# Optimization experiments

Measured on AMD Instinct MI355X. Metric: run time of the kernel, lower is better.

The kernel has to match this reference:

```python
import jax, jax.numpy as jnp
import numpy as np

N_NODES = 50000
N_EDGES = 800000
IN_DIM = 128
HID = 128
N_GRAPHS = 64


def _sage_conv(x, src, dst, Wl, bl, Wr):
    # PyG SAGEConv (mean aggr): out = lin_l(mean_{j in N(i)} x_j) + lin_r(x_i)
    msg = x[src]                                            # [E, d] gather
    agg = jax.ops.segment_sum(msg, dst, num_segments=N_NODES)   # [N, d]
    deg = jax.ops.segment_sum(jnp.ones((msg.shape[0],), x.dtype), dst,
                              num_segments=N_NODES)          # [N]
    agg = agg / jnp.clip(deg, 1.0, None)[:, None]            # mean (0 for isolated)
    return agg @ Wl.T + bl + x @ Wr.T


def setup_inputs() -> dict:
    key = jax.random.key(0)
    ks = jax.random.split(key, 12)
    x = jax.random.normal(ks[0], (N_NODES, IN_DIM), dtype=jnp.float32)
    edge_index = jax.random.randint(ks[1], (2, N_EDGES), 0, N_NODES, dtype=jnp.int64)
    batch = jnp.sort(jax.random.randint(ks[2], (N_NODES,), 0, N_GRAPHS, dtype=jnp.int64))
    def lin(k, out_d, in_d):
        s = 1.0 / np.sqrt(in_d)
        return jax.random.uniform(k, (out_d, in_d), jnp.float32, -s, s)
    inp = {"x": x, "edge_index": edge_index, "batch": batch}
    dims = [(IN_DIM, HID), (HID, HID), (HID, HID)]
    for l, (din, dout) in enumerate(dims):
        inp[f"Wl{l}"] = lin(ks[3 + 3 * l], dout, din)
        inp[f"bl{l}"] = jnp.zeros((dout,), jnp.float32)
        inp[f"Wr{l}"] = lin(ks[4 + 3 * l], dout, din)
    return inp


def reference(x, edge_index, batch, Wl0, bl0, Wr0, Wl1, bl1, Wr1, Wl2, bl2, Wr2):
    src, dst = edge_index[0], edge_index[1]
    h = jax.nn.relu(_sage_conv(x, src, dst, Wl0, bl0, Wr0))
    h = jax.nn.relu(_sage_conv(h, src, dst, Wl1, bl1, Wr1))
    h = _sage_conv(h, src, dst, Wl2, bl2, Wr2)
    # global_mean_pool: segment mean of node features by graph id
    s = jax.ops.segment_sum(h, batch, num_segments=N_GRAPHS)        # [G, d]
    cnt = jax.ops.segment_sum(jnp.ones((h.shape[0],), h.dtype), batch,
                              num_segments=N_GRAPHS)                 # [G]
    return s / jnp.clip(cnt, 1.0, None)[:, None]
```

## Files before the change

### kernel.cpp

```cpp
#include <hip/hip_runtime.h>

#define N_NODES 50000
#define N_EDGES 800000
#define DIM 128
#define KTOT 256
#define N_GRAPHS 64
#define BUCKET_CAP 64
#define LSTR 264

#define NBINS 391
#define BINCAP2 2816
#define N_NODES_PAD (NBINS * 128)

#define BIN1_TPB 512
#define BIN1_EPT 8
#define BIN1_EPB (BIN1_TPB * BIN1_EPT)
#define BIN1_GRID ((N_EDGES + BIN1_EPB - 1) / BIN1_EPB)

typedef __attribute__((ext_vector_type(8))) short bf16x8;
typedef __attribute__((ext_vector_type(16))) float f32x16;

__device__ __forceinline__ float bf2f(unsigned int u16) {
    return __uint_as_float(u16 << 16);
}
__device__ __forceinline__ unsigned short f2bf(float f) {
    unsigned int v = __float_as_uint(f);
    unsigned int r = (v + 0x7fffu + ((v >> 16) & 1u)) >> 16;
    return (unsigned short)r;
}

__global__ void castx_kernel(const float* __restrict__ x, ushort* __restrict__ xb,
                             int* __restrict__ bincnt) {
    int i = blockIdx.x * blockDim.x + threadIdx.x;
    if (i < NBINS) bincnt[i] = 0;
    if (i >= N_NODES * DIM / 4) return;
    float4 v = ((const float4*)x)[i];
    ushort4 o;
    o.x = f2bf(v.x); o.y = f2bf(v.y); o.z = f2bf(v.z); o.w = f2bf(v.w);
    ((ushort4*)xb)[i] = o;
}

__global__ void castw_kernel(const float* __restrict__ Wl0, const float* __restrict__ Wr0,
                             const float* __restrict__ Wl1, const float* __restrict__ Wr1,
                             const float* __restrict__ Wl2, const float* __restrict__ Wr2,
                             ushort* __restrict__ wb, float* __restrict__ pool) {
    int id = blockIdx.x * blockDim.x + threadIdx.x;
    if (id < N_GRAPHS * DIM) pool[id] = 0.f;
    if (id >= 3 * DIM * KTOT) return;
    int l = id >> 15;
    int r = id & 32767;
    int j = r >> 8, k = r & 255;
    const float* Wl = (l == 0) ? Wl0 : (l == 1) ? Wl1 : Wl2;
    const float* Wr = (l == 0) ? Wr0 : (l == 1) ? Wr1 : Wr2;
    float v = (k < DIM) ? Wl[j * DIM + k] : Wr[j * DIM + k - DIM];
    wb[id] = f2bf(v);
}

__global__ __launch_bounds__(BIN1_TPB) void bin1_kernel(
    const int* __restrict__ src, const int* __restrict__ dst,
    int* __restrict__ bincnt, uint* __restrict__ binbuf) {
    __shared__ uint hist[NBINS];
    __shared__ uint gbase[NBINS];
    const int tid = threadIdx.x;
    for (int i = tid; i < NBINS; i += BIN1_TPB) hist[i] = 0;
    __syncthreads();

    const int e0 = blockIdx.x * BIN1_EPB + tid * BIN1_EPT;
    uint val[BIN1_EPT];
    int  bin[BIN1_EPT];
    uint rk[BIN1_EPT];

    if (e0 + BIN1_EPT <= N_EDGES) {
        int4 s0 = *(const int4*)(src + e0);
        int4 s1 = *(const int4*)(src + e0 + 4);
        int4 d0 = *(const int4*)(dst + e0);
        int4 d1 = *(const int4*)(dst + e0 + 4);
        int ss[8] = {s0.x, s0.y, s0.z, s0.w, s1.x, s1.y, s1.z, s1.w};
        int dd[8] = {d0.x, d0.y, d0.z, d0.w, d1.x, d1.y, d1.z, d1.w};
        #pragma unroll
        for (int i = 0; i < BIN1_EPT; ++i) {
            bin[i] = dd[i] >> 7;
            val[i] = (uint)ss[i] | ((uint)(dd[i] & 127) << 16);
            rk[i]  = atomicAdd(&hist[bin[i]], 1u);
        }
    } else {
        #pragma unroll
        for (int i = 0; i < BIN1_EPT; ++i) {
            if (e0 + i < N_EDGES) {
                int s = src[e0 + i], d = dst[e0 + i];
                bin[i] = d >> 7;
                val[i] = (uint)s | ((uint)(d & 127) << 16);
                rk[i]  = atomicAdd(&hist[bin[i]], 1u);
            } else {
                bin[i] = -1; val[i] = 0; rk[i] = 0;
            }
        }
    }
    __syncthreads();

    for (int i = tid; i < NBINS; i += BIN1_TPB)
        gbase[i] = (uint)atomicAdd(&bincnt[i], (int)hist[i]);
    __syncthreads();

    #pragma unroll
    for (int i = 0; i < BIN1_EPT; ++i) {
        if (bin[i] >= 0) {
            uint pos = gbase[bin[i]] + rk[i];
            if (pos < BINCAP2)
                binbuf[(size_t)bin[i] * BINCAP2 + pos] = val[i];
        }
    }
}

__global__ __launch_bounds__(256) void bin2_kernel(
    const uint* __restrict__ binbuf, const int* __restrict__ bincnt,
    ushort* __restrict__ bucket, int* __restrict__ cnt) {
    __shared__ int lcnt[128];
    __shared__ ushort lbuck[128 * BUCKET_CAP];
    const int bin = blockIdx.x;
    const int tid = threadIdx.x;
    if (tid < 128) lcnt[tid] = 0;
    __syncthreads();
    int c = bincnt[bin];
    if (c > BINCAP2) c = BINCAP2;
    const uint* buf = binbuf + (size_t)bin * BINCAP2;
    for (int i = tid; i < c; i += 256) {
        uint v = buf[i];
        int ln = v >> 16;
        int pos = atomicAdd(&lcnt[ln], 1);
        if (pos < BUCKET_CAP) lbuck[ln * BUCKET_CAP + pos] = (ushort)(v & 0xffffu);
    }
    __syncthreads();
    const uint4* lb = (const uint4*)lbuck;
    uint4* gb = (uint4*)(bucket + (size_t)bin * 128 * BUCKET_CAP);
    #pragma unroll
    for (int i = tid; i < 128 * BUCKET_CAP / 8; i += 256)
        gb[i] = lb[i];
    if (tid < 128) cnt[bin * 128 + tid] = lcnt[tid];
}

template<int RELU, int POOL>
__global__ __launch_bounds__(512, 4) void layer_fused(
    const ushort* __restrict__ X, const int* __restrict__ cnt,
    const ushort* __restrict__ bucket, const ushort* __restrict__ wb,
    const float* __restrict__ bl, ushort* __restrict__ outb,
    const int* __restrict__ batch, float* __restrict__ pool)
{
    __shared__ ushort sA[64 * LSTR];
    const int tid = threadIdx.x;
    const int lane = tid & 63, w = tid >> 6;
    const int mh = w & 1, jq = w >> 1;
    const int n0 = blockIdx.x * 64;
    const int half = lane >> 5, lcol = lane & 31;

    #pragma unroll
    for (int it = 0; it < 2; ++it) {
        int ci = tid + it * 512;
        int row = ci >> 4;
        int k8 = (ci & 15) * 8;
        int gn = n0 + row;
        bf16x8 v = (bf16x8){0,0,0,0,0,0,0,0};
        if (gn < N_NODES) v = *(const bf16x8*)(X + (size_t)gn * DIM + k8);
        *(bf16x8*)(&sA[row * LSTR + DIM + k8]) = v;
    }

    for (int r8 = 0; r8 < 8; ++r8) {
        const int row = w * 8 + r8;
        const int gn = n0 + row;
        float a0 = 0.f, a1 = 0.f, a2 = 0.f, a3 = 0.f;
        int c = 0;
        if (gn < N_NODES) {
            c = cnt[gn];
            int cl = c < BUCKET_CAP ? c : BUCKET_CAP;
            const ushort* b = bucket + (size_t)gn * BUCKET_CAP;
            int e = half;
            for (; e + 6 < cl; e += 8) {
                int s0 = b[e], s1 = b[e + 2], s2 = b[e + 4], s3 = b[e + 6];
                uint2 u0 = *(const uint2*)(X + (size_t)s0 * DIM + lcol * 4);
                uint2 u1 = *(const uint2*)(X + (size_t)s1 * DIM + lcol * 4);
                uint2 u2 = *(const uint2*)(X + (size_t)s2 * DIM + lcol * 4);
                uint2 u3 = *(const uint2*)(X + (size_t)s3 * DIM + lcol * 4);
                a0 += bf2f(u0.x & 0xffff) + bf2f(u1.x & 0xffff) + bf2f(u2.x & 0xffff) + bf2f(u3.x & 0xffff);
                a1 += bf2f(u0.x >> 16)    + bf2f(u1.x >> 16)    + bf2f(u2.x >> 16)    + bf2f(u3.x >> 16);
                a2 += bf2f(u0.y & 0xffff) + bf2f(u1.y & 0xffff) + bf2f(u2.y & 0xffff) + bf2f(u3.y & 0xffff);
                a3 += bf2f(u0.y >> 16)    + bf2f(u1.y >> 16)    + bf2f(u2.y >> 16)    + bf2f(u3.y >> 16);
            }
            for (; e < cl; e += 2) {
                int s0 = b[e];
                uint2 u0 = *(const uint2*)(X + (size_t)s0 * DIM + lcol * 4);
                a0 += bf2f(u0.x & 0xffff);
                a1 += bf2f(u0.x >> 16);
                a2 += bf2f(u0.y & 0xffff);
                a3 += bf2f(u0.y >> 16);
            }
        }
        a0 += __shfl_xor(a0, 32);
        a1 += __shfl_xor(a1, 32);
        a2 += __shfl_xor(a2, 32);
        a3 += __shfl_xor(a3, 32);
        if (half == 0) {
            float inv = 1.0f / (float)(c > 0 ? c : 1);
            uint2 o;
            o.x = ((unsigned int)f2bf(a1 * inv) << 16) | f2bf(a0 * inv);
            o.y = ((unsigned int)f2bf(a3 * inv) << 16) | f2bf(a2 * inv);
            *(uint2*)(&sA[row * LSTR + lcol * 4]) = o;
        }
    }
    __syncthreads();

    bf16x8 bw[16];
    {
        const ushort* wp = wb + (size_t)(jq * 32 + (lane & 31)) * KTOT + (lane >> 5) * 8;
        #pragma unroll
        for (int kt = 0; kt < 16; ++kt)
            bw[kt] = *(const bf16x8*)(wp + kt * 16);
    }

    f32x16 acc = {};
    const int arow = mh * 32 + (lane & 31);
    const int akoff = (lane >> 5) * 8;
    #pragma unroll
    for (int kt = 0; kt < 16; ++kt) {
        bf16x8 a = *(const bf16x8*)(&sA[arow * LSTR + kt * 16 + akoff]);
        acc = __builtin_amdgcn_mfma_f32_32x32x16_bf16(a, bw[kt], acc, 0, 0, 0);
    }

    const int j = jq * 32 + (lane & 31);
    const float bias = bl[j];
    if (POOL) {
        float run = 0.f; int gcur = -1;
        #pragma unroll
        for (int r = 0; r < 16; ++r) {
            int row = (r & 3) + 8 * (r >> 2) + 4 * (lane >> 5);
            int gn = n0 + mh * 32 + row;
            if (gn < N_NODES) {
                float v = acc[r] + bias;
                int g = batch[gn];
                if (g != gcur) {
                    if (gcur >= 0) unsafeAtomicAdd(&pool[gcur * DIM + j], run);
                    run = 0.f; gcur = g;
                }
                run += v;
            }
        }
        if (gcur >= 0) unsafeAtomicAdd(&pool[gcur * DIM + j], run);
    } else {
        #pragma unroll
        for (int r = 0; r < 16; ++r) {
            int row = (r & 3) + 8 * (r >> 2) + 4 * (lane >> 5);
            int gn = n0 + mh * 32 + row;
            if (gn < N_NODES) {
                float v = acc[r] + bias;
                if (RELU) v = fmaxf(v, 0.f);
                outb[(size_t)gn * DIM + j] = f2bf(v);
            }
        }
    }
}

__global__ void pool2_kernel(const float* __restrict__ pool, const int* __restrict__ batch,
                             float* __restrict__ out) {
    int g = blockIdx.x;
    int j = threadIdx.x;
    int lo = 0, hi = N_NODES;
    while (lo < hi) { int m = (lo + hi) >> 1; if (batch[m] < g) lo = m + 1; else hi = m; }
    int start = lo;
    lo = start; hi = N_NODES;
    while (lo < hi) { int m = (lo + hi) >> 1; if (batch[m] < g + 1) lo = m + 1; else hi = m; }
    int cnt = lo - start;
    out[g * DIM + j] = pool[g * DIM + j] / (float)(cnt > 0 ? cnt : 1);
}

extern "C" void kernel_launch(void* const* d_in, const int* in_sizes, int n_in,
                              void* d_out, int out_size, void* d_ws, size_t ws_size,
                              hipStream_t stream) {
    const float* x    = (const float*)d_in[0];
    const int*   ei   = (const int*)d_in[1];
    const int*   src  = ei;
    const int*   dst  = ei + N_EDGES;
    const int*   batch = (const int*)d_in[2];
    const float* Wl0 = (const float*)d_in[3];
    const float* bl0 = (const float*)d_in[4];
    const float* Wr0 = (const float*)d_in[5];
    const float* Wl1 = (const float*)d_in[6];
    const float* bl1 = (const float*)d_in[7];
    const float* Wr1 = (const float*)d_in[8];
    const float* Wl2 = (const float*)d_in[9];
    const float* bl2 = (const float*)d_in[10];
    const float* Wr2 = (const float*)d_in[11];
    float* out = (float*)d_out;

    int*    cnt    = (int*)d_ws;
    ushort* bucket = (ushort*)(cnt + 65536);
    ushort* xb     = bucket + (size_t)N_NODES_PAD * BUCKET_CAP;
    ushort* h1b    = xb + (size_t)N_NODES * DIM;
    ushort* h2b    = h1b + (size_t)N_NODES * DIM;
    ushort* wb     = h2b + (size_t)N_NODES * DIM;
    float*  pool   = (float*)(wb + 3 * DIM * KTOT);
    int*    bincnt = (int*)(pool + N_GRAPHS * DIM);
    uint*   binbuf = (uint*)(bincnt + ((NBINS + 63) & ~63));

    castx_kernel<<<(N_NODES * DIM / 4 + 255) / 256, 256, 0, stream>>>(x, xb, bincnt);
    castw_kernel<<<(3 * DIM * KTOT + 255) / 256, 256, 0, stream>>>(Wl0, Wr0, Wl1, Wr1, Wl2, Wr2, wb, pool);
    bin1_kernel<<<BIN1_GRID, BIN1_TPB, 0, stream>>>(src, dst, bincnt, binbuf);
    bin2_kernel<<<NBINS, 256, 0, stream>>>(binbuf, bincnt, bucket, cnt);

    const int lgrid = (N_NODES + 63) / 64;
    layer_fused<1, 0><<<lgrid, 512, 0, stream>>>(xb,  cnt, bucket, wb,          bl0, h1b, batch, pool);
    layer_fused<1, 0><<<lgrid, 512, 0, stream>>>(h1b, cnt, bucket, wb + 32768,  bl1, h2b, batch, pool);
    layer_fused<0, 1><<<lgrid, 512, 0, stream>>>(h2b, cnt, bucket, wb + 65536,  bl2, nullptr, batch, pool);

    pool2_kernel<<<N_GRAPHS, DIM, 0, stream>>>(pool, batch, out);
}
```

Before: 273.3 us.

## Shrink layer tile to 32 nodes, prefetch bucket indices via shuffles

```diff
diff --git a/kernel.cpp b/kernel.cpp
--- a/kernel.cpp
+++ b/kernel.cpp
@@ -140,42 +140,46 @@
 }
 
 template<int RELU, int POOL>
-__global__ __launch_bounds__(512, 4) void layer_fused(
+__global__ __launch_bounds__(256, 8) void layer_fused(
     const ushort* __restrict__ X, const int* __restrict__ cnt,
     const ushort* __restrict__ bucket, const ushort* __restrict__ wb,
     const float* __restrict__ bl, ushort* __restrict__ outb,
     const int* __restrict__ batch, float* __restrict__ pool)
 {
-    __shared__ ushort sA[64 * LSTR];
+    __shared__ ushort sA[32 * LSTR];
     const int tid = threadIdx.x;
     const int lane = tid & 63, w = tid >> 6;
-    const int mh = w & 1, jq = w >> 1;
-    const int n0 = blockIdx.x * 64;
+    const int n0 = blockIdx.x * 32;
     const int half = lane >> 5, lcol = lane & 31;
 
-    #pragma unroll
-    for (int it = 0; it < 2; ++it) {
-        int ci = tid + it * 512;
-        int row = ci >> 4;
-        int k8 = (ci & 15) * 8;
-        int gn = n0 + row;
-        bf16x8 v = (bf16x8){0,0,0,0,0,0,0,0};
-        if (gn < N_NODES) v = *(const bf16x8*)(X + (size_t)gn * DIM + k8);
-        *(bf16x8*)(&sA[row * LSTR + DIM + k8]) = v;
-    }
-
-    for (int r8 = 0; r8 < 8; ++r8) {
-        const int row = w * 8 + r8;
-        const int gn = n0 + row;
-        float a0 = 0.f, a1 = 0.f, a2 = 0.f, a3 = 0.f;
-        int c = 0;
-        if (gn < N_NODES) {
-            c = cnt[gn];
-            int cl = c < BUCKET_CAP ? c : BUCKET_CAP;
-            const ushort* b = bucket + (size_t)gn * BUCKET_CAP;
-            int e = half;
-            for (; e + 6 < cl; e += 8) {
-                int s0 = b[e], s1 = b[e + 2], s2 = b[e + 4], s3 = b[e + 6];
+    const int sr0 = tid >> 4, sk0 = (tid & 15) * 8;
+    const int sr1 = sr0 + 16;
+    bf16x8 st0 = (bf16x8){0,0,0,0,0,0,0,0}, st1 = st0;
+    if (n0 + sr0 < N_NODES) st0 = *(const bf16x8*)(X + (size_t)(n0 + sr0) * DIM + sk0);
+    if (n0 + sr1 < N_NODES) st1 = *(const bf16x8*)(X + (size_t)(n0 + sr1) * DIM + sk0);
+
+    const int gn0 = n0 + w * 8;
+    int cw = cnt[gn0 + (lane & 7)];
+
+    for (int rp = 0; rp < 4; ++rp) {
+        int beL[2];
+        #pragma unroll
+        for (int q = 0; q < 2; ++q)
+            beL[q] = (int)bucket[(size_t)(gn0 + rp * 2 + q) * BUCKET_CAP + lane];
+        #pragma unroll
+        for (int q = 0; q < 2; ++q) {
+            const int r8 = rp * 2 + q;
+            const int row = w * 8 + r8;
+            const int c = __shfl(cw, r8);
+            const int cl = c < BUCKET_CAP ? c : BUCKET_CAP;
+            float a0 = 0.f, a1 = 0.f, a2 = 0.f, a3 = 0.f;
+            int t = 0;
+            for (; 2 * t + 7 < cl; t += 4) {
+                int e = 2 * t + half;
+                int s0 = __shfl(beL[q], e);
+                int s1 = __shfl(beL[q], e + 2);
+                int s2 = __shfl(beL[q], e + 4);
+                int s3 = __shfl(beL[q], e + 6);
                 uint2 u0 = *(const uint2*)(X + (size_t)s0 * DIM + lcol * 4);
                 uint2 u1 = *(const uint2*)(X + (size_t)s1 * DIM + lcol * 4);
                 uint2 u2 = *(const uint2*)(X + (size_t)s2 * DIM + lcol * 4);
@@ -185,54 +189,55 @@
                 a2 += bf2f(u0.y & 0xffff) + bf2f(u1.y & 0xffff) + bf2f(u2.y & 0xffff) + bf2f(u3.y & 0xffff);
                 a3 += bf2f(u0.y >> 16)    + bf2f(u1.y >> 16)    + bf2f(u2.y >> 16)    + bf2f(u3.y >> 16);
             }
-            for (; e < cl; e += 2) {
-                int s0 = b[e];
-                uint2 u0 = *(const uint2*)(X + (size_t)s0 * DIM + lcol * 4);
-                a0 += bf2f(u0.x & 0xffff);
-                a1 += bf2f(u0.x >> 16);
-                a2 += bf2f(u0.y & 0xffff);
-                a3 += bf2f(u0.y >> 16);
-            }
-        }
-        a0 += __shfl_xor(a0, 32);
-        a1 += __shfl_xor(a1, 32);
-        a2 += __shfl_xor(a2, 32);
-        a3 += __shfl_xor(a3, 32);
-        if (half == 0) {
-            float inv = 1.0f / (float)(c > 0 ? c : 1);
-            uint2 o;
-            o.x = ((unsigned int)f2bf(a1 * inv) << 16) | f2bf(a0 * inv);
-            o.y = ((unsigned int)f2bf(a3 * inv) << 16) | f2bf(a2 * inv);
-            *(uint2*)(&sA[row * LSTR + lcol * 4]) = o;
-        }
-    }
-    __syncthreads();
-
-    bf16x8 bw[16];
-    {
-        const ushort* wp = wb + (size_t)(jq * 32 + (lane & 31)) * KTOT + (lane >> 5) * 8;
-        #pragma unroll
-        for (int kt = 0; kt < 16; ++kt)
-            bw[kt] = *(const bf16x8*)(wp + kt * 16);
-    }
-
+            const int T = (cl + 1) >> 1;
+            for (; t < T; ++t) {
+                int e = 2 * t + half;
+                int s0 = __shfl(beL[q], e);
+                if (e < cl) {
+                    uint2 u0 = *(const uint2*)(X + (size_t)s0 * DIM + lcol * 4);
+                    a0 += bf2f(u0.x & 0xffff);
+                    a1 += bf2f(u0.x >> 16);
+                    a2 += bf2f(u0.y & 0xffff);
+                    a3 += bf2f(u0.y >> 16);
+                }
+            }
+            a0 += __shfl_xor(a0, 32);
+            a1 += __shfl_xor(a1, 32);
+            a2 += __shfl_xor(a2, 32);
+            a3 += __shfl_xor(a3, 32);
+            if (half == 0) {
+                float inv = 1.0f / (float)(c > 0 ? c : 1);
+                uint2 o;
+                o.x = ((unsigned int)f2bf(a1 * inv) << 16) | f2bf(a0 * inv);
+                o.y = ((unsigned int)f2bf(a3 * inv) << 16) | f2bf(a2 * inv);
+                *(uint2*)(&sA[row * LSTR + lcol * 4]) = o;
+            }
+        }
+    }
+
+    *(bf16x8*)(&sA[sr0 * LSTR + DIM + sk0]) = st0;
+    *(bf16x8*)(&sA[sr1 * LSTR + DIM + sk0]) = st1;
+    __syncthreads();
+
+    const ushort* wp = wb + (size_t)(w * 32 + (lane & 31)) * KTOT + (lane >> 5) * 8;
+    const int arow = lane & 31;
+    const int akoff = (lane >> 5) * 8;
     f32x16 acc = {};
-    const int arow = mh * 32 + (lane & 31);
-    const int akoff = (lane >> 5) * 8;
     #pragma unroll
     for (int kt = 0; kt < 16; ++kt) {
         bf16x8 a = *(const bf16x8*)(&sA[arow * LSTR + kt * 16 + akoff]);
-        acc = __builtin_amdgcn_mfma_f32_32x32x16_bf16(a, bw[kt], acc, 0, 0, 0);
-    }
-
-    const int j = jq * 32 + (lane & 31);
+        bf16x8 bwf = *(const bf16x8*)(wp + kt * 16);
+        acc = __builtin_amdgcn_mfma_f32_32x32x16_bf16(a, bwf, acc, 0, 0, 0);
+    }
+
+    const int j = w * 32 + (lane & 31);
     const float bias = bl[j];
     if (POOL) {
         float run = 0.f; int gcur = -1;
         #pragma unroll
         for (int r = 0; r < 16; ++r) {
             int row = (r & 3) + 8 * (r >> 2) + 4 * (lane >> 5);
-            int gn = n0 + mh * 32 + row;
+            int gn = n0 + row;
             if (gn < N_NODES) {
                 float v = acc[r] + bias;
                 int g = batch[gn];
@@ -248,7 +253,7 @@
         #pragma unroll
         for (int r = 0; r < 16; ++r) {
             int row = (r & 3) + 8 * (r >> 2) + 4 * (lane >> 5);
-            int gn = n0 + mh * 32 + row;
+            int gn = n0 + row;
             if (gn < N_NODES) {
                 float v = acc[r] + bias;
                 if (RELU) v = fmaxf(v, 0.f);
@@ -305,10 +310,10 @@
     bin1_kernel<<<BIN1_GRID, BIN1_TPB, 0, stream>>>(src, dst, bincnt, binbuf);
     bin2_kernel<<<NBINS, 256, 0, stream>>>(binbuf, bincnt, bucket, cnt);
 
-    const int lgrid = (N_NODES + 63) / 64;
-    layer_fused<1, 0><<<lgrid, 512, 0, stream>>>(xb,  cnt, bucket, wb,          bl0, h1b, batch, pool);
-    layer_fused<1, 0><<<lgrid, 512, 0, stream>>>(h1b, cnt, bucket, wb + 32768,  bl1, h2b, batch, pool);
-    layer_fused<0, 1><<<lgrid, 512, 0, stream>>>(h2b, cnt, bucket, wb + 65536,  bl2, nullptr, batch, pool);
+    const int lgrid = (N_NODES + 31) / 32;
+    layer_fused<1, 0><<<lgrid, 256, 0, stream>>>(xb,  cnt, bucket, wb,          bl0, h1b, batch, pool);
+    layer_fused<1, 0><<<lgrid, 256, 0, stream>>>(h1b, cnt, bucket, wb + 32768,  bl1, h2b, batch, pool);
+    layer_fused<0, 1><<<lgrid, 256, 0, stream>>>(h2b, cnt, bucket, wb + 65536,  bl2, nullptr, batch, pool);
 
     pool2_kernel<<<N_GRAPHS, DIM, 0, stream>>>(pool, batch, out);
 }
```

New measurement: 244.9 us. 1.12x faster.
